# Kernel optimization log

Measured on AMD Instinct MI355X. Metric: run time of the kernel, lower is better.

Reference implementation:

```python
import jax, jax.numpy as jnp
import numpy as np

NUM_LEVELS = 4
RADIUS = 4


def _bilinear_zeros(img, x, y):
    # img: (N, Hl, Wl); x, y: (N, K) pixel coords (align_corners=True identity map).
    # Replicates F.grid_sample(mode='bilinear', padding_mode='zeros', align_corners=True).
    N, Hl, Wl = img.shape
    x0 = jnp.floor(x); y0 = jnp.floor(y)
    wx1 = x - x0; wx0 = 1.0 - wx1
    wy1 = y - y0; wy0 = 1.0 - wy1
    bidx = jnp.arange(N)[:, None]

    def gather(xi, yi):
        inb = (xi >= 0) & (xi <= Wl - 1) & (yi >= 0) & (yi <= Hl - 1)
        xc = jnp.clip(xi, 0, Wl - 1).astype(jnp.int32)
        yc = jnp.clip(yi, 0, Hl - 1).astype(jnp.int32)
        vals = img[bidx, yc, xc]
        return jnp.where(inb, vals, jnp.zeros((), img.dtype))

    return (wy0 * wx0 * gather(x0, y0) + wy0 * wx1 * gather(x0 + 1, y0)
            + wy1 * wx0 * gather(x0, y0 + 1) + wy1 * wx1 * gather(x0 + 1, y0 + 1))


def setup_inputs() -> dict:
    key = jax.random.key(0)
    k1, k2, k3 = jax.random.split(key, 3)
    B, C, H, W = 2, 256, 64, 64
    fmap1 = jax.random.normal(k1, (B, C, H, W), dtype=jnp.float32)
    fmap2 = jax.random.normal(k2, (B, C, H, W), dtype=jnp.float32)
    # coords = base pixel grid + small random flow (stays mostly in-bounds)
    ys, xs = jnp.meshgrid(jnp.arange(H, dtype=jnp.float32), jnp.arange(W, dtype=jnp.float32), indexing='ij')
    grid = jnp.stack([xs, ys], axis=0)[None]  # (1, 2, H, W), channel0 = x
    flow = (jax.random.uniform(k3, (B, 2, H, W), dtype=jnp.float32) - 0.5) * 20.0
    coords = grid + flow
    return {'fmap1': fmap1, 'fmap2': fmap2, 'coords': coords}


def reference(fmap1, fmap2, coords):
    B, C, H, W = fmap1.shape
    HW = H * W
    # all-pairs correlation: (B, HW, HW), scaled by 1/sqrt(C)
    corr = jnp.einsum('bci,bcj->bij', fmap1.reshape(B, C, HW), fmap2.reshape(B, C, HW))
    corr = corr / jnp.sqrt(jnp.asarray(C, fmap1.dtype))
    corr = corr.reshape(B * HW, H, W)
    pyramid = [corr]
    for _ in range(NUM_LEVELS - 1):
        N, Hl, Wl = corr.shape
        corr = corr.reshape(N, Hl // 2, 2, Wl // 2, 2).mean(axis=(2, 4))  # avg_pool2d(2,2)
        pyramid.append(corr)

    r = RADIUS
    dy = jnp.linspace(-r, r, 2 * r + 1, dtype=coords.dtype)
    dx = jnp.linspace(-r, r, 2 * r + 1, dtype=coords.dtype)
    gy, gx = jnp.meshgrid(dy, dx, indexing='ij')  # matches torch.meshgrid(dy, dx)
    d0 = gy.reshape(-1); d1 = gx.reshape(-1)      # K = (2r+1)^2

    cperm = coords.transpose(0, 2, 3, 1).reshape(B * HW, 2)  # (N, 2), [:,0]=x, [:,1]=y
    outs = []
    for i, corr_l in enumerate(pyramid):
        cl = cperm / (2.0 ** i)
        # coords_lvl = centroid + delta; xgrid uses delta[...,0]=dy grid, ygrid uses delta[...,1]=dx grid
        x = cl[:, 0:1] + d0[None, :]
        y = cl[:, 1:2] + d1[None, :]
        outs.append(_bilinear_zeros(corr_l, x, y))  # (N, K)
    out = jnp.concatenate(outs, axis=-1)            # (N, num_levels*K)
    out = out.reshape(B, H, W, -1).transpose(0, 3, 1, 2)  # (B, 324, H, W)
    return out
```

## Files before the change

### kernel.cpp

```cpp
#include <hip/hip_runtime.h>
#include <cstdint>

#define B2 2
#define CCH 256
#define HH 64
#define WW 64
#define HWHW 4096
#define KOUT 324

typedef _Float16 half_t;
typedef _Float16 h2 __attribute__((ext_vector_type(2)));
typedef _Float16 h8 __attribute__((ext_vector_type(8)));
typedef float f32x4 __attribute__((ext_vector_type(4)));

__device__ __forceinline__ float fdot2f(h2 a, h2 b, float c) {
#if __has_builtin(__builtin_amdgcn_fdot2)
  return __builtin_amdgcn_fdot2(a, b, c, false);
#else
  return c + (float)a.x * (float)b.x + (float)a.y * (float)b.y;
#endif
}

__global__ __launch_bounds__(256) void transpose_cl(
    const float* __restrict__ f1, const float* __restrict__ f2,
    half_t* __restrict__ f1t, half_t* __restrict__ f2t) {
  __shared__ float tile[32][33];
  int zz = blockIdx.z;
  const float* src = (zz < 2) ? f1 : f2;
  half_t* dst = (zz < 2) ? f1t : f2t;
  float s = (zz < 2) ? 0.0625f : 1.0f;
  int b = zz & 1;
  int hw0 = blockIdx.x * 32;
  int c0 = blockIdx.y * 32;
  int tx = threadIdx.x;
  int ty = threadIdx.y;
  const float* sb = src + (size_t)b * CCH * HWHW;
  half_t* db = dst + (size_t)b * HWHW * CCH;
#pragma unroll
  for (int i = 0; i < 4; i++)
    tile[ty + i * 8][tx] = sb[(size_t)(c0 + ty + i * 8) * HWHW + hw0 + tx];
  __syncthreads();
#pragma unroll
  for (int i = 0; i < 4; i++)
    db[(size_t)(hw0 + ty + i * 8) * CCH + c0 + tx] = (half_t)(tile[tx][ty + i * 8] * s);
}

__global__ __launch_bounds__(256) void pool_all(
    const h2* __restrict__ l0, h2* __restrict__ l1,
    h2* __restrict__ l2, h2* __restrict__ l3) {
  int idx = blockIdx.x * blockDim.x + threadIdx.x;
  const int n1 = B2 * 32 * 32 * 128;
  const int n2 = B2 * 16 * 16 * 128;
  const int n3 = B2 * 8 * 8 * 128;
  int L, Wo, local;
  h2* dst;
  if (idx < n1) { L = 1; Wo = 32; local = idx; dst = l1; }
  else if (idx < n1 + n2) { L = 2; Wo = 16; local = idx - n1; dst = l2; }
  else if (idx < n1 + n2 + n3) { L = 3; Wo = 8; local = idx - n1 - n2; dst = l3; }
  else return;
  int f = 1 << L;
  int sh = 6 - L;
  int c2 = local & 127;
  int t = local >> 7;
  int x = t & (Wo - 1);
  int y = (t >> sh) & (Wo - 1);
  int b = t >> (2 * sh);
  const h2* src = l0 + (size_t)b * HWHW * 128 + c2;
  float ax = 0.f, ay = 0.f;
  for (int dy = 0; dy < f; dy++)
    for (int dx = 0; dx < f; dx++) {
      h2 a = src[(size_t)((y * f + dy) * WW + (x * f + dx)) * 128];
      ax += (float)a.x; ay += (float)a.y;
    }
  float s = 1.0f / (float)(f * f);
  h2 r;
  r.x = (half_t)(ax * s);
  r.y = (half_t)(ay * s);
  dst[local] = r;
}

__global__ __launch_bounds__(256) void corr23_k(
    const half_t* __restrict__ f1t,
    const half_t* __restrict__ f2l2, const half_t* __restrict__ f2l3,
    float* __restrict__ corr) {
  int bid = blockIdx.x;
  int g = ((bid & 7) << 6) | (bid >> 3);
  int n0 = g << 4;
  int b = n0 >> 12;
  int w = threadIdx.x >> 6;
  int l = threadIdx.x & 63;
  int row = l & 15;
  int kg = l >> 4;

  const h8* A = (const h8*)(f1t + ((size_t)(n0 + row) * CCH) + kg * 8);
  h8 a[8];
#pragma unroll
  for (int ks = 0; ks < 8; ks++) a[ks] = A[ks * 4];

  for (int nt = w * 5; nt < w * 5 + 5; nt++) {
    const half_t* Bb = (nt < 16)
        ? f2l2 + ((size_t)b * 256 + nt * 16) * CCH
        : f2l3 + ((size_t)b * 64 + (nt - 16) * 16) * CCH;
    const h8* Bp = (const h8*)(Bb + (size_t)row * CCH + kg * 8);
    f32x4 acc = {0.f, 0.f, 0.f, 0.f};
#pragma unroll
    for (int ks = 0; ks < 8; ks++)
      acc = __builtin_amdgcn_mfma_f32_16x16x32_f16(a[ks], Bp[ks * 4], acc, 0, 0, 0);
#pragma unroll
    for (int r = 0; r < 4; r++) {
      int q = kg * 4 + r;
      corr[(size_t)(n0 + q) * 320 + nt * 16 + row] = acc[r];
    }
  }
}

__device__ __forceinline__ float dpp_sum16(float x) {
  int v;
  v = __builtin_amdgcn_update_dpp(0, __float_as_int(x), 0xB1, 0xF, 0xF, true);
  x += __int_as_float(v);
  v = __builtin_amdgcn_update_dpp(0, __float_as_int(x), 0x4E, 0xF, 0xF, true);
  x += __int_as_float(v);
  v = __builtin_amdgcn_update_dpp(0, __float_as_int(x), 0x141, 0xF, 0xF, true);
  x += __int_as_float(v);
  v = __builtin_amdgcn_update_dpp(0, __float_as_int(x), 0x140, 0xF, 0xF, true);
  x += __int_as_float(v);
  return x;
}

__global__ __launch_bounds__(512, 4) void sample16b(
    const float* __restrict__ coords,
    const half_t* __restrict__ f1t,
    const half_t* __restrict__ f2l0, const half_t* __restrict__ f2l1,
    const float* __restrict__ corr,
    float* __restrict__ out) {
  __shared__ float4 f1s4[512];
  __shared__ float P[2][16][100];
  __shared__ float wgt[2][16][4];
  __shared__ float cxy[2][16];

  int bid = blockIdx.x;
  int g = ((bid & 7) << 6) | (bid >> 3);
  int n0 = g << 4;
  int b = n0 >> 12;
  int i0 = n0 & 4095;
  int yi = i0 >> 6;
  int x0 = i0 & 63;
  int tid = threadIdx.x;

  f1s4[tid] = ((const float4*)(f1t + (size_t)n0 * CCH))[tid];
  if (tid < 32) {
    int q = tid & 15, c = tid >> 4;
    cxy[c][q] = coords[(size_t)(b * 2 + c) * HWHW + i0 + q];
  }
  __syncthreads();

  int w = tid >> 6;
  int l = w >> 2;
  int lane = tid & 63;
  int lg = lane >> 4;
  int l16 = lane & 15;

  float inv = (l == 0) ? 1.0f : 0.5f;
  int Hl = HH >> l, Wl = WW >> l;
  const half_t* f2 = (l == 0) ? f2l0 : f2l1;
  const float4* f2b = (const float4*)(f2) + (size_t)b * Hl * Wl * 32 + l16;
  const h2* f1h = (const h2*)f1s4;

  for (int qq = 0; qq < 4; qq++) {
    int q = (w & 3) * 4 + qq;
    float clx = cxy[0][q], cly = cxy[1][q];
    float xl = clx * inv, yl = cly * inv;
    float fx = floorf(xl), fy = floorf(yl);
    int ix0 = (int)fx - 4, iy0 = (int)fy - 4;
    float wx1 = xl - fx, wy1 = yl - fy;
    if (lane == 0) {
      wgt[l][q][0] = 1.0f - wx1; wgt[l][q][1] = wx1;
      wgt[l][q][2] = 1.0f - wy1; wgt[l][q][3] = wy1;
    }
    int fi = q * 128 + l16 * 4;
    h2 fa0 = f1h[fi + 0], fa1 = f1h[fi + 1], fa2 = f1h[fi + 2], fa3 = f1h[fi + 3];
    h2 fb0 = f1h[fi + 64], fb1 = f1h[fi + 65], fb2 = f1h[fi + 66], fb3 = f1h[fi + 67];

    int u = 0, v = lg, t = lg;
    for (int it = 0; it < 25; it++) {
      int txp = ix0 + u, typ = iy0 + v;
      bool inb = ((unsigned)txp < (unsigned)Wl) & ((unsigned)typ < (unsigned)Hl);
      float d = 0.0f;
      if (inb) {
        const float4* tp = f2b + (size_t)(typ * Wl + txp) * 32;
        float4 A = tp[0];
        float4 Bv = tp[16];
        const h2* ah = (const h2*)&A;
        const h2* bh = (const h2*)&Bv;
        d = fdot2f(ah[0], fa0, d); d = fdot2f(ah[1], fa1, d);
        d = fdot2f(ah[2], fa2, d); d = fdot2f(ah[3], fa3, d);
        d = fdot2f(bh[0], fb0, d); d = fdot2f(bh[1], fb1, d);
        d = fdot2f(bh[2], fb2, d); d = fdot2f(bh[3], fb3, d);
      }
      d = dpp_sum16(d);
      if (l16 == 0) P[l][q][t] = d;
      t += 4; v += 4;
      bool wrap = v >= 10;
      v = wrap ? v - 10 : v;
      u = wrap ? u + 1 : u;
    }
  }
  __syncthreads();

#pragma unroll
  for (int it = 0; it < 6; it++) {
    int kidx = it * 32 + (tid >> 4);
    if (kidx < 162) {
      int lvl = kidx >= 81;
      int k = kidx - 81 * lvl;
      int q = tid & 15;
      int a = k / 9, bb2 = k - a * 9;
      float wx0 = wgt[lvl][q][0], wx1 = wgt[lvl][q][1];
      float wy0 = wgt[lvl][q][2], wy1 = wgt[lvl][q][3];
      const float* Pq = P[lvl][q];
      float val = wy0 * (wx0 * Pq[a * 10 + bb2] + wx1 * Pq[(a + 1) * 10 + bb2])
                + wy1 * (wx0 * Pq[a * 10 + bb2 + 1] + wx1 * Pq[(a + 1) * 10 + bb2 + 1]);
      out[(size_t)(b * KOUT + lvl * 81 + k) * HWHW + (size_t)yi * WW + x0 + q] = val;
    }
  }

#pragma unroll
  for (int it = 0; it < 6; it++) {
    int kidx = it * 32 + (tid >> 4);
    if (kidx < 162) {
      int lvl = 2 + (kidx >= 81);
      int k = kidx - 81 * (kidx >= 81);
      int q = tid & 15;
      float inv2 = (lvl == 2) ? 0.25f : 0.125f;
      int Wl2 = (lvl == 2) ? 16 : 8;
      int base = (lvl == 2) ? 0 : 256;
      float xl = cxy[0][q] * inv2, yl = cxy[1][q] * inv2;
      float fx = floorf(xl), fy = floorf(yl);
      int ix0 = (int)fx - 4, iy0 = (int)fy - 4;
      float wx1 = xl - fx, wx0 = 1.0f - wx1;
      float wy1 = yl - fy, wy0 = 1.0f - wy1;
      const float* cq = corr + (size_t)(n0 + q) * 320 + base;
      int a = k / 9, bb2 = k - a * 9;
      float p00 = 0.f, p10 = 0.f, p01 = 0.f, p11 = 0.f;
      {
        int x = ix0 + a, y = iy0 + bb2;
        if (((unsigned)x < (unsigned)Wl2) & ((unsigned)y < (unsigned)Wl2)) p00 = cq[y * Wl2 + x];
      }
      {
        int x = ix0 + a + 1, y = iy0 + bb2;
        if (((unsigned)x < (unsigned)Wl2) & ((unsigned)y < (unsigned)Wl2)) p10 = cq[y * Wl2 + x];
      }
      {
        int x = ix0 + a, y = iy0 + bb2 + 1;
        if (((unsigned)x < (unsigned)Wl2) & ((unsigned)y < (unsigned)Wl2)) p01 = cq[y * Wl2 + x];
      }
      {
        int x = ix0 + a + 1, y = iy0 + bb2 + 1;
        if (((unsigned)x < (unsigned)Wl2) & ((unsigned)y < (unsigned)Wl2)) p11 = cq[y * Wl2 + x];
      }
      float val = wy0 * (wx0 * p00 + wx1 * p10) + wy1 * (wx0 * p01 + wx1 * p11);
      out[(size_t)(b * KOUT + lvl * 81 + k) * HWHW + (size_t)yi * WW + x0 + q] = val;
    }
  }
}

extern "C" void kernel_launch(void* const* d_in, const int* in_sizes, int n_in,
                              void* d_out, int out_size, void* d_ws, size_t ws_size,
                              hipStream_t stream) {
  const float* fmap1 = (const float*)d_in[0];
  const float* fmap2 = (const float*)d_in[1];
  const float* coords = (const float*)d_in[2];
  float* out = (float*)d_out;

  char* ws = (char*)d_ws;
  half_t* f1t  = (half_t*)(ws);
  half_t* f2l0 = (half_t*)(ws + ((size_t)4 << 20));
  half_t* f2l1 = (half_t*)(ws + ((size_t)8 << 20));
  half_t* f2l2 = (half_t*)(ws + ((size_t)9 << 20));
  half_t* f2l3 = (half_t*)(ws + ((size_t)9 << 20) + ((size_t)512 << 10));
  float*  corr = (float*)(ws + ((size_t)10 << 20));

  dim3 tb(32, 8, 1);
  dim3 tg(HWHW / 32, CCH / 32, 4);
  transpose_cl<<<tg, tb, 0, stream>>>(fmap1, fmap2, f1t, f2l0);

  int npool = B2 * (32 * 32 + 16 * 16 + 8 * 8) * 128;
  pool_all<<<(npool + 255) / 256, 256, 0, stream>>>(
      (const h2*)f2l0, (h2*)f2l1, (h2*)f2l2, (h2*)f2l3);

  corr23_k<<<512, 256, 0, stream>>>(f1t, f2l2, f2l3, corr);

  sample16b<<<512, 512, 0, stream>>>(coords, f1t, f2l0, f2l1, corr, out);
}
```

Measured before the change: 147.8 us.

## Zero-pad level-0/1 feature maps and sample two pixels per wave

Levels 0 and 1 of fmap2 are stored in zero-padded buffers (16-pixel border), so the correlation lookup needs no bounds checks and steps through memory with incremental offsets. The sampling kernel now handles 8 pixels per block across 1024 blocks. Each wave computes two pixels at once, which doubles the independent loads and dot products in flight. In exchange, a new kernel zeroes about 13.6 MB of workspace on every call, and the padded level-0 buffer is larger, which adds memory traffic and one more launch.

```diff
diff --git a/kernel.cpp b/kernel.cpp
--- a/kernel.cpp
+++ b/kernel.cpp
@@ -13,6 +13,9 @@
 typedef _Float16 h8 __attribute__((ext_vector_type(8)));
 typedef float f32x4 __attribute__((ext_vector_type(4)));
 
+#define P0 96
+#define P1 64
+
 __device__ __forceinline__ float fdot2f(h2 a, h2 b, float c) {
 #if __has_builtin(__builtin_amdgcn_fdot2)
   return __builtin_amdgcn_fdot2(a, b, c, false);
@@ -21,13 +24,17 @@
 #endif
 }
 
+__global__ __launch_bounds__(256) void zero_pads(float4* __restrict__ p, int n) {
+  int i = blockIdx.x * 256 + threadIdx.x;
+  if (i < n) p[i] = make_float4(0.f, 0.f, 0.f, 0.f);
+}
+
 __global__ __launch_bounds__(256) void transpose_cl(
     const float* __restrict__ f1, const float* __restrict__ f2,
-    half_t* __restrict__ f1t, half_t* __restrict__ f2t) {
+    half_t* __restrict__ f1t, half_t* __restrict__ f2l0p) {
   __shared__ float tile[32][33];
   int zz = blockIdx.z;
   const float* src = (zz < 2) ? f1 : f2;
-  half_t* dst = (zz < 2) ? f1t : f2t;
   float s = (zz < 2) ? 0.0625f : 1.0f;
   int b = zz & 1;
   int hw0 = blockIdx.x * 32;
@@ -35,28 +42,37 @@
   int tx = threadIdx.x;
   int ty = threadIdx.y;
   const float* sb = src + (size_t)b * CCH * HWHW;
-  half_t* db = dst + (size_t)b * HWHW * CCH;
 #pragma unroll
   for (int i = 0; i < 4; i++)
     tile[ty + i * 8][tx] = sb[(size_t)(c0 + ty + i * 8) * HWHW + hw0 + tx];
   __syncthreads();
-#pragma unroll
-  for (int i = 0; i < 4; i++)
-    db[(size_t)(hw0 + ty + i * 8) * CCH + c0 + tx] = (half_t)(tile[tx][ty + i * 8] * s);
+  if (zz < 2) {
+    half_t* db = f1t + (size_t)b * HWHW * CCH;
+#pragma unroll
+    for (int i = 0; i < 4; i++)
+      db[(size_t)(hw0 + ty + i * 8) * CCH + c0 + tx] = (half_t)(tile[tx][ty + i * 8] * s);
+  } else {
+    half_t* db = f2l0p + (size_t)b * P0 * P0 * CCH;
+#pragma unroll
+    for (int i = 0; i < 4; i++) {
+      int hw = hw0 + ty + i * 8;
+      int y = hw >> 6, x = hw & 63;
+      db[(size_t)((y + 16) * P0 + (x + 16)) * CCH + c0 + tx] = (half_t)tile[tx][ty + i * 8];
+    }
+  }
 }
 
 __global__ __launch_bounds__(256) void pool_all(
-    const h2* __restrict__ l0, h2* __restrict__ l1,
+    const h2* __restrict__ l0p, h2* __restrict__ l1p,
     h2* __restrict__ l2, h2* __restrict__ l3) {
   int idx = blockIdx.x * blockDim.x + threadIdx.x;
   const int n1 = B2 * 32 * 32 * 128;
   const int n2 = B2 * 16 * 16 * 128;
   const int n3 = B2 * 8 * 8 * 128;
   int L, Wo, local;
-  h2* dst;
-  if (idx < n1) { L = 1; Wo = 32; local = idx; dst = l1; }
-  else if (idx < n1 + n2) { L = 2; Wo = 16; local = idx - n1; dst = l2; }
-  else if (idx < n1 + n2 + n3) { L = 3; Wo = 8; local = idx - n1 - n2; dst = l3; }
+  if (idx < n1) { L = 1; Wo = 32; local = idx; }
+  else if (idx < n1 + n2) { L = 2; Wo = 16; local = idx - n1; }
+  else if (idx < n1 + n2 + n3) { L = 3; Wo = 8; local = idx - n1 - n2; }
   else return;
   int f = 1 << L;
   int sh = 6 - L;
@@ -65,18 +81,23 @@
   int x = t & (Wo - 1);
   int y = (t >> sh) & (Wo - 1);
   int b = t >> (2 * sh);
-  const h2* src = l0 + (size_t)b * HWHW * 128 + c2;
+  const h2* src = l0p + (size_t)b * P0 * P0 * 128 + c2;
   float ax = 0.f, ay = 0.f;
   for (int dy = 0; dy < f; dy++)
     for (int dx = 0; dx < f; dx++) {
-      h2 a = src[(size_t)((y * f + dy) * WW + (x * f + dx)) * 128];
+      h2 a = src[(size_t)((y * f + dy + 16) * P0 + (x * f + dx + 16)) * 128];
       ax += (float)a.x; ay += (float)a.y;
     }
   float s = 1.0f / (float)(f * f);
   h2 r;
   r.x = (half_t)(ax * s);
   r.y = (half_t)(ay * s);
-  dst[local] = r;
+  if (L == 1)
+    l1p[((size_t)b * P1 * P1 + (size_t)(y + 16) * P1 + (x + 16)) * 128 + c2] = r;
+  else if (L == 2)
+    l2[local] = r;
+  else
+    l3[local] = r;
 }
 
 __global__ __launch_bounds__(256) void corr23_k(
@@ -127,93 +148,109 @@
   return x;
 }
 
-__global__ __launch_bounds__(512, 4) void sample16b(
+__global__ __launch_bounds__(512, 8) void sample8(
     const float* __restrict__ coords,
     const half_t* __restrict__ f1t,
-    const half_t* __restrict__ f2l0, const half_t* __restrict__ f2l1,
+    const half_t* __restrict__ f2l0p, const half_t* __restrict__ f2l1p,
     const float* __restrict__ corr,
     float* __restrict__ out) {
-  __shared__ float4 f1s4[512];
-  __shared__ float P[2][16][100];
-  __shared__ float wgt[2][16][4];
-  __shared__ float cxy[2][16];
+  __shared__ float4 f1s4[256];
+  __shared__ float P[2][8][100];
+  __shared__ float wgt[2][8][4];
+  __shared__ float cxy[2][8];
 
   int bid = blockIdx.x;
-  int g = ((bid & 7) << 6) | (bid >> 3);
-  int n0 = g << 4;
+  int g = ((bid & 7) << 7) | (bid >> 3);
+  int n0 = g << 3;
   int b = n0 >> 12;
   int i0 = n0 & 4095;
   int yi = i0 >> 6;
   int x0 = i0 & 63;
   int tid = threadIdx.x;
 
-  f1s4[tid] = ((const float4*)(f1t + (size_t)n0 * CCH))[tid];
-  if (tid < 32) {
-    int q = tid & 15, c = tid >> 4;
+  if (tid < 256) f1s4[tid] = ((const float4*)(f1t + (size_t)n0 * CCH))[tid];
+  if (tid < 16) {
+    int q = tid & 7, c = tid >> 3;
     cxy[c][q] = coords[(size_t)(b * 2 + c) * HWHW + i0 + q];
   }
   __syncthreads();
 
   int w = tid >> 6;
   int l = w >> 2;
+  int p = w & 3;
   int lane = tid & 63;
   int lg = lane >> 4;
   int l16 = lane & 15;
 
+  int Pl = (l == 0) ? P0 : P1;
   float inv = (l == 0) ? 1.0f : 0.5f;
-  int Hl = HH >> l, Wl = WW >> l;
-  const half_t* f2 = (l == 0) ? f2l0 : f2l1;
-  const float4* f2b = (const float4*)(f2) + (size_t)b * Hl * Wl * 32 + l16;
+  const float4* f2b = (l == 0)
+      ? (const float4*)f2l0p + ((size_t)b * P0 * P0 + 16 * P0 + 16) * 32 + l16
+      : (const float4*)f2l1p + ((size_t)b * P1 * P1 + 16 * P1 + 16) * 32 + l16;
   const h2* f1h = (const h2*)f1s4;
 
-  for (int qq = 0; qq < 4; qq++) {
-    int q = (w & 3) * 4 + qq;
-    float clx = cxy[0][q], cly = cxy[1][q];
-    float xl = clx * inv, yl = cly * inv;
-    float fx = floorf(xl), fy = floorf(yl);
-    int ix0 = (int)fx - 4, iy0 = (int)fy - 4;
-    float wx1 = xl - fx, wy1 = yl - fy;
-    if (lane == 0) {
-      wgt[l][q][0] = 1.0f - wx1; wgt[l][q][1] = wx1;
-      wgt[l][q][2] = 1.0f - wy1; wgt[l][q][3] = wy1;
-    }
-    int fi = q * 128 + l16 * 4;
-    h2 fa0 = f1h[fi + 0], fa1 = f1h[fi + 1], fa2 = f1h[fi + 2], fa3 = f1h[fi + 3];
-    h2 fb0 = f1h[fi + 64], fb1 = f1h[fi + 65], fb2 = f1h[fi + 66], fb3 = f1h[fi + 67];
-
-    int u = 0, v = lg, t = lg;
-    for (int it = 0; it < 25; it++) {
-      int txp = ix0 + u, typ = iy0 + v;
-      bool inb = ((unsigned)txp < (unsigned)Wl) & ((unsigned)typ < (unsigned)Hl);
-      float d = 0.0f;
-      if (inb) {
-        const float4* tp = f2b + (size_t)(typ * Wl + txp) * 32;
-        float4 A = tp[0];
-        float4 Bv = tp[16];
-        const h2* ah = (const h2*)&A;
-        const h2* bh = (const h2*)&Bv;
-        d = fdot2f(ah[0], fa0, d); d = fdot2f(ah[1], fa1, d);
-        d = fdot2f(ah[2], fa2, d); d = fdot2f(ah[3], fa3, d);
-        d = fdot2f(bh[0], fb0, d); d = fdot2f(bh[1], fb1, d);
-        d = fdot2f(bh[2], fb2, d); d = fdot2f(bh[3], fb3, d);
-      }
-      d = dpp_sum16(d);
-      if (l16 == 0) P[l][q][t] = d;
-      t += 4; v += 4;
-      bool wrap = v >= 10;
-      v = wrap ? v - 10 : v;
-      u = wrap ? u + 1 : u;
-    }
+  int q0 = 2 * p, q1 = 2 * p + 1;
+  float xl0 = cxy[0][q0] * inv, yl0 = cxy[1][q0] * inv;
+  float xl1 = cxy[0][q1] * inv, yl1 = cxy[1][q1] * inv;
+  float fx0 = floorf(xl0), fy0 = floorf(yl0);
+  float fx1 = floorf(xl1), fy1 = floorf(yl1);
+  int ix00 = (int)fx0 - 4, iy00 = (int)fy0 - 4;
+  int ix01 = (int)fx1 - 4, iy01 = (int)fy1 - 4;
+  if (lane == 0) {
+    wgt[l][q0][0] = 1.0f - (xl0 - fx0); wgt[l][q0][1] = xl0 - fx0;
+    wgt[l][q0][2] = 1.0f - (yl0 - fy0); wgt[l][q0][3] = yl0 - fy0;
+    wgt[l][q1][0] = 1.0f - (xl1 - fx1); wgt[l][q1][1] = xl1 - fx1;
+    wgt[l][q1][2] = 1.0f - (yl1 - fy1); wgt[l][q1][3] = yl1 - fy1;
+  }
+
+  int fi0 = q0 * 128 + l16 * 4;
+  h2 a00 = f1h[fi0], a01 = f1h[fi0 + 1], a02 = f1h[fi0 + 2], a03 = f1h[fi0 + 3];
+  h2 a04 = f1h[fi0 + 64], a05 = f1h[fi0 + 65], a06 = f1h[fi0 + 66], a07 = f1h[fi0 + 67];
+  int fi1 = q1 * 128 + l16 * 4;
+  h2 a10 = f1h[fi1], a11 = f1h[fi1 + 1], a12 = f1h[fi1 + 2], a13 = f1h[fi1 + 3];
+  h2 a14 = f1h[fi1 + 64], a15 = f1h[fi1 + 65], a16 = f1h[fi1 + 66], a17 = f1h[fi1 + 67];
+
+  int v = lg, t = lg;
+  int off0 = (iy00 + lg) * Pl + ix00;
+  int off1 = (iy01 + lg) * Pl + ix01;
+  const int dP = 4 * Pl;
+  const int dW = 1 - 10 * Pl;
+  for (int it = 0; it < 25; it++) {
+    const float4* tp0 = f2b + (ptrdiff_t)off0 * 32;
+    const float4* tp1 = f2b + (ptrdiff_t)off1 * 32;
+    float4 A0 = tp0[0];
+    float4 B0 = tp0[16];
+    float4 A1 = tp1[0];
+    float4 B1 = tp1[16];
+    const h2* ah0 = (const h2*)&A0;
+    const h2* bh0 = (const h2*)&B0;
+    const h2* ah1 = (const h2*)&A1;
+    const h2* bh1 = (const h2*)&B1;
+    float d0 = 0.f, d1 = 0.f;
+    d0 = fdot2f(ah0[0], a00, d0); d0 = fdot2f(ah0[1], a01, d0);
+    d0 = fdot2f(ah0[2], a02, d0); d0 = fdot2f(ah0[3], a03, d0);
+    d0 = fdot2f(bh0[0], a04, d0); d0 = fdot2f(bh0[1], a05, d0);
+    d0 = fdot2f(bh0[2], a06, d0); d0 = fdot2f(bh0[3], a07, d0);
+    d1 = fdot2f(ah1[0], a10, d1); d1 = fdot2f(ah1[1], a11, d1);
+    d1 = fdot2f(ah1[2], a12, d1); d1 = fdot2f(ah1[3], a13, d1);
+    d1 = fdot2f(bh1[0], a14, d1); d1 = fdot2f(bh1[1], a15, d1);
+    d1 = fdot2f(bh1[2], a16, d1); d1 = fdot2f(bh1[3], a17, d1);
+    d0 = dpp_sum16(d0);
+    d1 = dpp_sum16(d1);
+    if (l16 == 0) { P[l][q0][t] = d0; P[l][q1][t] = d1; }
+    t += 4; v += 4;
+    off0 += dP; off1 += dP;
+    if (v >= 10) { v -= 10; off0 += dW; off1 += dW; }
   }
   __syncthreads();
 
 #pragma unroll
-  for (int it = 0; it < 6; it++) {
-    int kidx = it * 32 + (tid >> 4);
+  for (int it = 0; it < 3; it++) {
+    int kidx = it * 64 + (tid >> 3);
     if (kidx < 162) {
       int lvl = kidx >= 81;
       int k = kidx - 81 * lvl;
-      int q = tid & 15;
+      int q = tid & 7;
       int a = k / 9, bb2 = k - a * 9;
       float wx0 = wgt[lvl][q][0], wx1 = wgt[lvl][q][1];
       float wy0 = wgt[lvl][q][2], wy1 = wgt[lvl][q][3];
@@ -225,12 +262,12 @@
   }
 
 #pragma unroll
-  for (int it = 0; it < 6; it++) {
-    int kidx = it * 32 + (tid >> 4);
+  for (int it = 0; it < 3; it++) {
+    int kidx = it * 64 + (tid >> 3);
     if (kidx < 162) {
       int lvl = 2 + (kidx >= 81);
       int k = kidx - 81 * (kidx >= 81);
-      int q = tid & 15;
+      int q = tid & 7;
       float inv2 = (lvl == 2) ? 0.25f : 0.125f;
       int Wl2 = (lvl == 2) ? 16 : 8;
       int base = (lvl == 2) ? 0 : 256;
@@ -273,22 +310,25 @@
   float* out = (float*)d_out;
 
   char* ws = (char*)d_ws;
-  half_t* f1t  = (half_t*)(ws);
-  half_t* f2l0 = (half_t*)(ws + ((size_t)4 << 20));
-  half_t* f2l1 = (half_t*)(ws + ((size_t)8 << 20));
-  half_t* f2l2 = (half_t*)(ws + ((size_t)9 << 20));
-  half_t* f2l3 = (half_t*)(ws + ((size_t)9 << 20) + ((size_t)512 << 10));
-  float*  corr = (float*)(ws + ((size_t)10 << 20));
+  half_t* f1t   = (half_t*)(ws);
+  half_t* f2l0p = (half_t*)(ws + 4194304);
+  half_t* f2l1p = (half_t*)(ws + 13631488);
+  half_t* f2l2  = (half_t*)(ws + 17825792);
+  half_t* f2l3  = (half_t*)(ws + 18087936);
+  float*  corr  = (float*)(ws + 18153472);
+
+  int nz = 13631488 / 16;
+  zero_pads<<<nz / 256, 256, 0, stream>>>((float4*)f2l0p, nz);
 
   dim3 tb(32, 8, 1);
   dim3 tg(HWHW / 32, CCH / 32, 4);
-  transpose_cl<<<tg, tb, 0, stream>>>(fmap1, fmap2, f1t, f2l0);
+  transpose_cl<<<tg, tb, 0, stream>>>(fmap1, fmap2, f1t, f2l0p);
 
   int npool = B2 * (32 * 32 + 16 * 16 + 8 * 8) * 128;
   pool_all<<<(npool + 255) / 256, 256, 0, stream>>>(
-      (const h2*)f2l0, (h2*)f2l1, (h2*)f2l2, (h2*)f2l3);
+      (const h2*)f2l0p, (h2*)f2l1p, (h2*)f2l2, (h2*)f2l3);
 
   corr23_k<<<512, 256, 0, stream>>>(f1t, f2l2, f2l3, corr);
 
-  sample16b<<<512, 512, 0, stream>>>(coords, f1t, f2l0, f2l1, corr, out);
-}
+  sample8<<<1024, 512, 0, stream>>>(coords, f1t, f2l0p, f2l1p, corr, out);
+}
```

Measured after the change: 145.4 us. About the same (-1.6%).
